# Performance work log

Hardware: AMD Instinct MI355X
Metric: run time of the kernel (lower is better)

Reference implementation:

```python
import jax, jax.numpy as jnp
import numpy as np
from jax import lax

S = 16  # encoder stride (patchify-conv stand-in for the CNN backbone, stride-16 feature grid)


def _conv(x, w, b, stride, padding):
    y = lax.conv_general_dilated(x, w, (stride, stride), padding,
                                 dimension_numbers=('NCHW', 'OIHW', 'NCHW'))
    return y + b[None, :, None, None]


def _l2norm(x, eps=1e-12):  # F.normalize(p=2, dim=1)
    n = jnp.sqrt(jnp.sum(x * x, axis=1, keepdims=True))
    return x / jnp.maximum(n, eps)


def _encode(frame, ew, eb, kw, kb, vw, vb, mask=None):
    feat = jax.nn.relu(_conv(frame, ew, eb, S, 'VALID'))  # [B,512,h,w]
    key = _conv(feat, kw, kb, 1, 'SAME')                  # [B,64,h,w]
    val = _conv(feat, vw, vb, 1, 'SAME')                  # [B,ed,h,w]
    if mask is not None:
        m = mask[:, None, ::S, ::S]  # torch F.interpolate 'nearest' with exact integer factor
        key = key * m
        val = val * m
    return _l2norm(key), val, feat


def _forward(query_frame, prev_frame, prev_mask, first_frame, first_mask,
             enc_q_w, enc_q_b, enc_m_w, enc_m_b,
             key_w, key_b, val_w, val_b,
             dec1_w, dec1_b, dec2_w, dec2_b, cls_w, cls_b):
    # memory bank reset + push(first), push(prev)
    k1, v1, _ = _encode(first_frame, enc_m_w, enc_m_b, key_w, key_b, val_w, val_b, first_mask)
    kp, vp, _ = _encode(prev_frame, enc_m_w, enc_m_b, key_w, key_b, val_w, val_b, prev_mask)
    qk, qv, _ = _encode(query_frame, enc_q_w, enc_q_b, key_w, key_b, val_w, val_b)
    B, Ck, h, w = qk.shape
    ed = qv.shape[1]
    mem_key = jnp.concatenate([k1.reshape(B, Ck, -1), kp.reshape(B, Ck, -1)], axis=2)  # [B,64,M]
    mem_val = jnp.concatenate([v1.reshape(B, ed, -1), vp.reshape(B, ed, -1)], axis=2)  # [B,ed,M]
    q_key = qk.reshape(B, Ck, -1)                                                      # [B,64,Q]
    # STM memory read: affinity -> softmax -> weighted sum over memory pixels
    affinity = jnp.einsum('bcq,bcm->bqm', q_key, mem_key) / jnp.sqrt(jnp.float32(Ck))
    affinity = jax.nn.softmax(affinity, axis=-1)
    mem_read = jnp.einsum('bqm,bcm->bcq', affinity, mem_val).reshape(B, ed, h, w)
    fused = jnp.concatenate([qv, mem_read], axis=1)  # [B,2*ed,h,w] (aspp=False)
    d = jax.nn.relu(_conv(fused, dec1_w, dec1_b, 1, 'SAME'))
    dec_feat = jax.nn.relu(_conv(d, dec2_w, dec2_b, 1, 'SAME'))
    logits = _conv(dec_feat, cls_w, cls_b, 1, 'SAME')
    H, W = query_frame.shape[-2], query_frame.shape[-1]
    logits_full = jax.image.resize(logits, (B, logits.shape[1], H, W), method='bilinear')  # align_corners=False
    rep_feat = _l2norm(dec_feat)
    return rep_feat, logits_full


def setup_inputs():
    key = jax.random.key(0)
    ks = jax.random.split(key, 16)
    B, H, W = 8, 512, 512
    Ce, Ck, ed = 512, 64, 256
    g = lambda i, sh, s: jax.random.normal(ks[i], sh, dtype=jnp.float32) * s
    return {
        'query_frame': g(0, (B, 3, H, W), 1.0),
        'prev_frame': g(1, (B, 3, H, W), 1.0),
        'prev_mask': jnp.round(jax.random.uniform(ks[2], (B, H, W), dtype=jnp.float32)),
        'first_frame': g(3, (B, 3, H, W), 1.0),
        'first_mask': jnp.round(jax.random.uniform(ks[4], (B, H, W), dtype=jnp.float32)),
        'enc_q_w': g(5, (Ce, 3, S, S), 0.02), 'enc_q_b': jnp.zeros((Ce,), jnp.float32),
        'enc_m_w': g(6, (Ce, 3, S, S), 0.02), 'enc_m_b': jnp.zeros((Ce,), jnp.float32),
        'key_w': g(7, (Ck, Ce, 1, 1), 0.05), 'key_b': jnp.zeros((Ck,), jnp.float32),
        'val_w': g(8, (ed, Ce, 1, 1), 0.05), 'val_b': jnp.zeros((ed,), jnp.float32),
        'dec1_w': g(9, (ed, 2 * ed, 3, 3), 0.02), 'dec1_b': jnp.zeros((ed,), jnp.float32),
        'dec2_w': g(10, (ed, ed, 3, 3), 0.02), 'dec2_b': jnp.zeros((ed,), jnp.float32),
        'cls_w': g(11, (2, ed, 1, 1), 0.05), 'cls_b': jnp.zeros((2,), jnp.float32),
    }


def reference(query_frame, prev_frame, prev_mask, first_frame, first_mask,
              enc_q_w, enc_q_b, enc_m_w, enc_m_b,
              key_w, key_b, val_w, val_b,
              dec1_w, dec1_b, dec2_w, dec2_b, cls_w, cls_b):
    return _forward(query_frame, prev_frame, prev_mask, first_frame, first_mask,
                    enc_q_w, enc_q_b, enc_m_w, enc_m_b,
                    key_w, key_b, val_w, val_b,
                    dec1_w, dec1_b, dec2_w, dec2_b, cls_w, cls_b)
```

## Files before the change

kernel.cpp:

```cpp
#include <hip/hip_runtime.h>
#include <hip/hip_bf16.h>
#include <cstdint>

#define DEV __device__ __forceinline__
typedef __attribute__((ext_vector_type(8))) short short8;
typedef __attribute__((ext_vector_type(4))) float f32x4;
typedef unsigned short u16;

DEV float b2f(u16 u) { union { unsigned int i; float f; } x; x.i = (unsigned)u << 16; return x.f; }
DEV u16 f2b(float f) { __hip_bfloat16 h = __float2bfloat16(f); return *(u16*)&h; }
DEV float rdin(const void* p, size_t i, int isbf) {
  return isbf ? __bfloat162float(((const __hip_bfloat16*)p)[i]) : ((const float*)p)[i];
}
DEV void wrout(void* p, size_t i, float v, int isbf) {
  if (isbf) ((__hip_bfloat16*)p)[i] = __float2bfloat16(v);
  else      ((float*)p)[i] = v;
}
DEV short8 ld8(const void* p, size_t idx, int isbf) {
  if (isbf) return *(const short8*)((const u16*)p + idx);
  const float* f = (const float*)p + idx;
  float4 x = *(const float4*)f, y = *(const float4*)(f + 4);
  short8 r;
  r[0] = f2b(x.x); r[1] = f2b(x.y); r[2] = f2b(x.z); r[3] = f2b(x.w);
  r[4] = f2b(y.x); r[5] = f2b(y.y); r[6] = f2b(y.z); r[7] = f2b(y.w);
  return r;
}
DEV void gl16(const u16* g, u16* l) {
  __builtin_amdgcn_global_load_lds(
      (const __attribute__((address_space(1))) void*)g,
      (__attribute__((address_space(3))) void*)l, 16, 0, 0);
}
DEV void bar() {
  asm volatile("" ::: "memory");
  __builtin_amdgcn_s_barrier();
  asm volatile("" ::: "memory");
}

__global__ __launch_bounds__(256) void detect_k(const u16* w, int* flag) {
  __shared__ int cnt[256];
  int tid = threadIdx.x, c = 0;
  for (int i = tid; i < 4096; i += 256) {
    u16 v = w[i];
    int e = (v >> 7) & 0xFF;
    if (v == 0 || (e >= 0x60 && e <= 0x9F)) c++;
  }
  cnt[tid] = c;
  __syncthreads();
  for (int s = 128; s > 0; s >>= 1) { if (tid < s) cnt[tid] += cnt[tid + s]; __syncthreads(); }
  if (tid == 0) *flag = (cnt[0] > 3600) ? 1 : 0;
}

__global__ __launch_bounds__(256) void patchify_k(const void* F0, const void* F1,
                                                  u16* dst, const int* dflag) {
  int isbf = *dflag;
  int bid = blockIdx.x;
  int z = bid >> 8, rem = bid & 255, b = rem >> 5, y = rem & 31;
  const void* F = z ? F1 : F0;
  int x = threadIdx.x & 31, pj = threadIdx.x >> 5;
  u16* drow = dst + (size_t)(z * 8192 + b * 1024 + y * 32 + x) * 768;
#pragma unroll
  for (int i = 0; i < 6; i++) {
    int pair = i * 8 + pj;
    int c = pair >> 4, ky = pair & 15;
    size_t src = ((size_t)((b * 3 + c) * 512 + y * 16 + ky)) * 512 + x * 16;
    short8 v0 = ld8(F, src, isbf);
    short8 v1 = ld8(F, src + 8, isbf);
    u16* dp = drow + c * 256 + ky * 16;
    *(short8*)dp = v0;
    *(short8*)(dp + 8) = v1;
  }
}

__global__ __launch_bounds__(256) void wconv_k(const void* wm, const void* wq,
                                               u16* dst, float* rsum, const int* dflag) {
  int isbf = *dflag;
  int gi = blockIdx.x * 256 + threadIdx.x;
  if (gi < 8192) rsum[gi] = 0.f;
  size_t e0 = (size_t)gi * 8;
  const void* src = e0 < 393216 ? wm : wq;
  size_t off = e0 < 393216 ? e0 : e0 - 393216;
  *(short8*)&dst[e0] = ld8(src, off, isbf);
}

__global__ __launch_bounds__(256) void kvconv_k(const void* valW, const void* keyW,
                                                u16* dst, const int* dflag) {
  int isbf = *dflag;
  int idx = blockIdx.x * 256 + threadIdx.x;
  size_t e0 = (size_t)idx * 8;
  int row = (int)(e0 >> 9);
  const void* src = row < 256 ? valW : keyW;
  size_t off = row < 256 ? e0 : e0 - (size_t)256 * 512;
  *(short8*)&dst[e0] = ld8(src, off, isbf);
}

struct PA {
  const void* W0; const void* W1; size_t bs; int K; int rowsplit; int zsel; int ws16; int rowmax1;
  DEV short8 l8(int row, int k, int b, int zz, int isbf) const {
    const void* W = W0; int r = row;
    if (zsel && zz == 2) W = W1;
    else if (rowsplit && row >= rowsplit) { W = W1; r = row - rowsplit; if (r > rowmax1) r = rowmax1; }
    return ld8(W, (size_t)b * bs + (size_t)r * K + k, ws16 ? 1 : isbf);
  }
  DEV const u16* ga(int row, int k, int b, int zz) const {
    int r = row; if (rowsplit && r > rowmax1) r = rowmax1;
    return (const u16*)W0 + (size_t)b * bs + (size_t)r * K + k;
  }
};
struct PBws {
  const u16* X; int rs; size_t zs;
  DEV short8 l8(int t, int k, int zz, int) const {
    return *(const short8*)(X + (size_t)zz * zs + (size_t)t * rs + k);
  }
  DEV const u16* ga(int t, int k, int zz) const {
    return X + (size_t)zz * zs + (size_t)t * rs + k;
  }
};
struct PBc3 {
  const u16* X; int C; int shift;
  DEV short8 l8(int t, int k, int, int) const {
    int tap = k >> shift, c0 = k & (C - 1);
    int dy = tap / 3, dx = tap - dy * 3;
    int pos = t & 1023, y = pos >> 5, x = pos & 31;
    int iy = y + dy - 1, ix = x + dx - 1;
    if ((unsigned)iy >= 32u || (unsigned)ix >= 32u) { short8 z = {0,0,0,0,0,0,0,0}; return z; }
    return *(const short8*)(X + (size_t)(((t >> 10) * 1024) + iy * 32 + ix) * C + c0);
  }
};

struct Epi {
  int mode;
  u16 *o16, *o16b, *o16c;
  size_t zs; int ts, moff, mmax;
  const void *bias, *bias2; int bzsel;
  const void *maskA, *maskB;
  const float* rscale;
  float scale; int relu, doexp;
  float* rsum;
  int rinv;
  DEV void store1(int m, int t, int z, float v, int isbf) const {
    if (m >= mmax) return;
    int b = t >> 10, pos = t & 1023;
    if (m < 256) {
      v += rdin(bias, m, isbf);
      if (z < 2) {
        const void* mk = z ? maskB : maskA;
        v *= rdin(mk, ((size_t)(b * 512 + (pos >> 5) * 16) << 9) + (pos & 31) * 16, isbf);
        o16[((size_t)(b * 256 + m)) * 2048 + (size_t)z * 1024 + pos] = f2b(v);
      } else {
        o16b[(size_t)t * 512 + m] = f2b(v);
      }
    } else {
      v += rdin(bias2, m - 256, isbf);
      o16c[((size_t)z * 8192 + t) * 64 + (m - 256)] = f2b(v);
    }
  }
};

DEV void epilogue(const Epi& ep, f32x4 (&acc)[4][4], u16* sh, int isbf, int tid,
                  int col16, int quad, int wm, int wn, int zz, int m0, int n0, int nbase) {
  if (ep.mode == 1) {
#pragma unroll
    for (int mt = 0; mt < 4; mt++)
#pragma unroll
      for (int nt = 0; nt < 4; nt++)
#pragma unroll
        for (int r = 0; r < 4; r++) {
          int m = m0 + wm * 64 + mt * 16 + quad * 4 + r;
          int t = nbase + n0 + wn * 64 + nt * 16 + col16;
          ep.store1(m, t, zz, acc[mt][nt][r], isbf);
        }
    return;
  }
  if (ep.mode == 2) {
    float* pf = (float*)ep.o16;
#pragma unroll
    for (int mt = 0; mt < 4; mt++)
#pragma unroll
      for (int nt = 0; nt < 4; nt++)
#pragma unroll
        for (int r = 0; r < 4; r++) {
          int m = m0 + wm * 64 + mt * 16 + quad * 4 + r;
          int t = nbase + n0 + wn * 64 + nt * 16 + col16;
          pf[((size_t)(zz * 256 + m)) * 8192 + t] = acc[mt][nt][r];
        }
    return;
  }
  u16* T = sh;
  const int TS = 132;
  for (int p = 0; p < 2; p++) {
    __syncthreads();
    if (wn == p) {
      float tsum[4] = {0.f, 0.f, 0.f, 0.f};
#pragma unroll
      for (int mt = 0; mt < 4; mt++)
#pragma unroll
        for (int nt = 0; nt < 4; nt++) {
          int tl = nt * 16 + col16;
          int tg = nbase + n0 + p * 64 + tl;
#pragma unroll
          for (int r2 = 0; r2 < 2; r2++) {
            int ml = wm * 64 + mt * 16 + quad * 4 + r2 * 2;
            float v0 = acc[mt][nt][r2 * 2] * ep.scale;
            float v1 = acc[mt][nt][r2 * 2 + 1] * ep.scale;
            if (ep.bias) {
              const void* bp = (ep.bzsel && zz == 2) ? ep.bias2 : ep.bias;
              v0 += rdin(bp, m0 + ml, isbf);
              v1 += rdin(bp, m0 + ml + 1, isbf);
            }
            if (ep.doexp) { v0 = __expf(v0); v1 = __expf(v1); }
            if (ep.rscale) {
              float rs = ep.rscale[tg];
              if (ep.rinv) rs = 1.f / rs;
              v0 *= rs; v1 *= rs;
            }
            if (ep.relu) { v0 = fmaxf(v0, 0.f); v1 = fmaxf(v1, 0.f); }
            if (ep.rsum) tsum[nt] += v0 + v1;
            unsigned int pk = (unsigned)f2b(v0) | ((unsigned)f2b(v1) << 16);
            *(unsigned int*)&T[tl * TS + ml] = pk;
          }
        }
      if (ep.rsum) {
#pragma unroll
        for (int nt = 0; nt < 4; nt++)
          atomicAdd(&ep.rsum[nbase + n0 + p * 64 + nt * 16 + col16], tsum[nt]);
      }
    }
    __syncthreads();
    {
      int tl = tid >> 2, seg = tid & 3;
      int tg = nbase + n0 + p * 64 + tl;
      u16* op = ep.o16 + (size_t)zz * ep.zs + (size_t)tg * ep.ts + ep.moff + m0;
#pragma unroll
      for (int i = 0; i < 4; i++) {
        int c8 = seg + i * 4;
        short8 v = *(short8*)&T[tl * TS + c8 * 8];
        *(short8*)&op[c8 * 8] = v;
      }
    }
  }
}

template <class PB>
__global__ __launch_bounds__(256) void mgl(PA pa, PB pb, Epi ep, int ktiles, int nbase,
                                           const int* dflag) {
  __shared__ u16 sh[32768];
  int isbf = *dflag;
  int tid = threadIdx.x, lane = tid & 63;
  int col16 = lane & 15, quad = lane >> 4;
  int wv = tid >> 6, wm = wv >> 1, wn = wv & 1;
  int zz = blockIdx.z;
  int n0 = blockIdx.x * 128, m0 = blockIdx.y * 128;
  int bA = (nbase + n0) >> 10;

  f32x4 acc[4][4];
#pragma unroll
  for (int mt = 0; mt < 4; mt++)
#pragma unroll
    for (int nt = 0; nt < 4; nt++)
#pragma unroll
      for (int r = 0; r < 4; r++) acc[mt][nt][r] = 0.f;

  int rA[4], lA[4];
#pragma unroll
  for (int g = 0; g < 4; g++) {
    rA[g] = g * 32 + (tid >> 3);
    lA[g] = (tid & 7) ^ (rA[g] & 7);
  }

  auto issue = [&](int kt) {
    int kk = kt * 64;
    u16* base = sh + ((kt & 1) << 14);
#pragma unroll
    for (int g = 0; g < 4; g++) {
      gl16(pa.ga(m0 + rA[g], kk + lA[g] * 8, bA, zz), base + (size_t)(g * 256 + tid) * 8);
      gl16(pb.ga(nbase + n0 + rA[g], kk + lA[g] * 8, zz), base + 8192 + (size_t)(g * 256 + tid) * 8);
    }
  };
  issue(0);

  for (int kt = 0; kt < ktiles; kt++) {
    const u16* As = sh + ((kt & 1) << 14);
    const u16* Bs = As + 8192;
    if (kt + 1 < ktiles) {
      issue(kt + 1);
      asm volatile("s_waitcnt vmcnt(8)" ::: "memory");
    } else {
      asm volatile("s_waitcnt vmcnt(0)" ::: "memory");
    }
    bar();
#pragma unroll
    for (int s = 0; s < 2; s++) {
      short8 af[4], bf[4];
      int cs = ((s * 4 + quad) ^ (col16 & 7)) << 3;
#pragma unroll
      for (int mt = 0; mt < 4; mt++)
        af[mt] = *(const short8*)&As[(wm * 64 + mt * 16 + col16) * 64 + cs];
#pragma unroll
      for (int nt = 0; nt < 4; nt++)
        bf[nt] = *(const short8*)&Bs[(wn * 64 + nt * 16 + col16) * 64 + cs];
#pragma unroll
      for (int mt = 0; mt < 4; mt++)
#pragma unroll
        for (int nt = 0; nt < 4; nt++)
          acc[mt][nt] = __builtin_amdgcn_mfma_f32_16x16x32_bf16(af[mt], bf[nt], acc[mt][nt], 0, 0, 0);
    }
    bar();
  }

  epilogue(ep, acc, sh, isbf, tid, col16, quad, wm, wn, zz, m0, n0, nbase);
}

template <class PB>
__global__ __launch_bounds__(256) void mg(PA pa, PB pb, Epi ep, int ktiles, int nbase,
                                          int ksplit, const int* dflag) {
  __shared__ u16 sh[32768];
  int isbf = *dflag;
  int tid = threadIdx.x, lane = tid & 63;
  int col16 = lane & 15, quad = lane >> 4;
  int wv = tid >> 6, wm = wv >> 1, wn = wv & 1;
  int zz = blockIdx.z;
  int kb = ksplit * zz;
  int n0 = blockIdx.x * 128, m0 = blockIdx.y * 128;
  int bA = (nbase + n0) >> 10;

  f32x4 acc[4][4];
#pragma unroll
  for (int mt = 0; mt < 4; mt++)
#pragma unroll
    for (int nt = 0; nt < 4; nt++)
#pragma unroll
      for (int r = 0; r < 4; r++) acc[mt][nt][r] = 0.f;

  int rA[4], lA[4];
#pragma unroll
  for (int g = 0; g < 4; g++) {
    rA[g] = g * 32 + (tid >> 3);
    lA[g] = (tid & 7) ^ (rA[g] & 7);
  }

  short8 ra[4], rb[4];
#pragma unroll
  for (int g = 0; g < 4; g++) {
    ra[g] = pa.l8(m0 + rA[g], kb + lA[g] * 8, bA, zz, isbf);
    rb[g] = pb.l8(nbase + n0 + rA[g], kb + lA[g] * 8, zz, isbf);
  }
#pragma unroll
  for (int g = 0; g < 4; g++) {
    *(short8*)&sh[(size_t)(g * 256 + tid) * 8] = ra[g];
    *(short8*)&sh[8192 + (size_t)(g * 256 + tid) * 8] = rb[g];
  }
  __syncthreads();

  for (int kt = 0; kt < ktiles; kt++) {
    const u16* As = sh + ((kt & 1) ? 16384 : 0);
    const u16* Bs = As + 8192;
    bool more = (kt + 1 < ktiles);
    if (more) {
      int kn = kb + (kt + 1) * 64;
#pragma unroll
      for (int g = 0; g < 4; g++) {
        ra[g] = pa.l8(m0 + rA[g], kn + lA[g] * 8, bA, zz, isbf);
        rb[g] = pb.l8(nbase + n0 + rA[g], kn + lA[g] * 8, zz, isbf);
      }
    }
#pragma unroll
    for (int s = 0; s < 2; s++) {
      short8 af[4], bf[4];
      int cs = ((s * 4 + quad) ^ (col16 & 7)) << 3;
#pragma unroll
      for (int mt = 0; mt < 4; mt++)
        af[mt] = *(const short8*)&As[(wm * 64 + mt * 16 + col16) * 64 + cs];
#pragma unroll
      for (int nt = 0; nt < 4; nt++)
        bf[nt] = *(const short8*)&Bs[(wn * 64 + nt * 16 + col16) * 64 + cs];
#pragma unroll
      for (int mt = 0; mt < 4; mt++)
#pragma unroll
        for (int nt = 0; nt < 4; nt++)
          acc[mt][nt] = __builtin_amdgcn_mfma_f32_16x16x32_bf16(af[mt], bf[nt], acc[mt][nt], 0, 0, 0);
    }
    if (more) {
      u16* An = sh + (!(kt & 1) ? 16384 : 0);
#pragma unroll
      for (int g = 0; g < 4; g++) {
        *(short8*)&An[(size_t)(g * 256 + tid) * 8] = ra[g];
        *(short8*)&An[8192 + (size_t)(g * 256 + tid) * 8] = rb[g];
      }
      __syncthreads();
    }
  }

  epilogue(ep, acc, sh, isbf, tid, col16, quad, wm, wn, zz, m0, n0, nbase);
}

__global__ __launch_bounds__(256) void comb_k(const float* pf, const void* bias,
                                              u16* out, int ts, int moff, int npart,
                                              int relu, const float* rsum,
                                              const int* dflag) {
  int isbf = *dflag;
  int tid = threadIdx.x;
  int t = blockIdx.x * 64 + (tid & 63);
  int m = blockIdx.y * 8 + ((tid >> 6) << 1);
  float rs = rsum ? 1.f / rsum[t] : 1.f;
  float v0 = 0.f, v1 = 0.f;
  for (int p = 0; p < npart; p++) {
    v0 += pf[(size_t)(p * 256 + m) * 8192 + t];
    v1 += pf[(size_t)(p * 256 + m + 1) * 8192 + t];
  }
  v0 *= rs; v1 *= rs;
  if (bias) { v0 += rdin(bias, m, isbf); v1 += rdin(bias, m + 1, isbf); }
  if (relu) { v0 = fmaxf(v0, 0.f); v1 = fmaxf(v1, 0.f); }
  unsigned int pk = (unsigned)f2b(v0) | ((unsigned)f2b(v1) << 16);
  *(unsigned int*)&out[(size_t)t * ts + moff + m] = pk;
}

__global__ __launch_bounds__(256) void wreorder_k(const void* src, u16* dst, int C,
                                                  int total, const int* dflag) {
  int idx = blockIdx.x * 256 + threadIdx.x;
  if (idx >= total) return;
  int isbf = *dflag;
  int nine_c = 9 * C;
  int m = idx / nine_c; int r = idx - m * nine_c;
  int tp = r / C; int c = r - tp * C;
  dst[idx] = f2b(rdin(src, (size_t)(m * C + c) * 9 + tp, isbf));
}

__global__ __launch_bounds__(256) void keyfix_k(const u16* kraw3, const void* mA,
                                                const void* mB, u16* memk, u16* qk,
                                                const int* dflag) {
  int isbf = *dflag;
  int z = blockIdx.y;
  int n = blockIdx.x * 256 + threadIdx.x;
  int b = n >> 10, pos = n & 1023;
  float mv = 1.f;
  if (z == 0) mv = rdin(mA, ((size_t)(b * 512 + (pos >> 5) * 16) << 9) + (pos & 31) * 16, isbf);
  else if (z == 1) mv = rdin(mB, ((size_t)(b * 512 + (pos >> 5) * 16) << 9) + (pos & 31) * 16, isbf);
  const u16* src = kraw3 + ((size_t)z * 8192 + n) * 64;
  float v[64], ss = 0.f;
#pragma unroll
  for (int c = 0; c < 64; c++) { v[c] = b2f(src[c]) * mv; ss += v[c] * v[c]; }
  float inv = 1.f / fmaxf(sqrtf(ss), 1e-12f);
  u16* dst = (z < 2) ? memk + (size_t)(b * 2048 + z * 1024 + pos) * 64 : qk + (size_t)n * 64;
#pragma unroll
  for (int c = 0; c < 64; c++) dst[c] = f2b(v[c] * inv);
}

__global__ __launch_bounds__(256) void repcls_k(const u16* decf, const void* cwgt,
                                                const void* cbias, void* out_rep,
                                                float* logits, const int* dflag) {
  int isbf = *dflag;
  int tid = threadIdx.x, lane = tid & 63, wv = tid >> 6;
  int tok = blockIdx.x * 4 + wv;
  int b = tok >> 10, pos = tok & 1023;
  const u16* src = decf + (size_t)tok * 256;
  int c0 = lane * 4;
  float v[4], ss = 0.f, a0 = 0.f, a1 = 0.f;
#pragma unroll
  for (int j = 0; j < 4; j++) {
    float x = b2f(src[c0 + j]);
    v[j] = x; ss += x * x;
    a0 = fmaf(x, rdin(cwgt, c0 + j, isbf), a0);
    a1 = fmaf(x, rdin(cwgt, 256 + c0 + j, isbf), a1);
  }
#pragma unroll
  for (int off = 32; off > 0; off >>= 1) {
    ss += __shfl_down(ss, off); a0 += __shfl_down(a0, off); a1 += __shfl_down(a1, off);
  }
  ss = __shfl(ss, 0); a0 = __shfl(a0, 0); a1 = __shfl(a1, 0);
  float inv = 1.f / fmaxf(sqrtf(ss), 1e-12f);
#pragma unroll
  for (int j = 0; j < 4; j++)
    wrout(out_rep, ((size_t)(b * 256 + c0 + j) << 10) + pos, v[j] * inv, isbf);
  if (lane == 0) {
    logits[((size_t)(b * 2) << 10) + pos]     = a0 + rdin(cbias, 0, isbf);
    logits[((size_t)(b * 2 + 1) << 10) + pos] = a1 + rdin(cbias, 1, isbf);
  }
}

__global__ __launch_bounds__(256) void resize_k(const float* logits, void* out,
                                                size_t ebase, const int* dflag) {
  int isbf = *dflag;
  int idx = blockIdx.x * 256 + threadIdx.x;
  int ox = idx & 511, oy = (idx >> 9) & 511, c = (idx >> 18) & 1, b = idx >> 19;
  float fy = (oy + 0.5f) * 0.0625f - 0.5f;
  float fx = (ox + 0.5f) * 0.0625f - 0.5f;
  int y0 = (int)floorf(fy), x0 = (int)floorf(fx);
  float wy = fy - y0, wx = fx - x0;
  int y0c = max(y0, 0), y1c = min(y0 + 1, 31);
  int x0c = max(x0, 0), x1c = min(x0 + 1, 31);
  const float* L = logits + ((size_t)(b * 2 + c) << 10);
  float v00 = L[y0c * 32 + x0c], v01 = L[y0c * 32 + x1c];
  float v10 = L[y1c * 32 + x0c], v11 = L[y1c * 32 + x1c];
  float v = (1.f - wy) * ((1.f - wx) * v00 + wx * v01) + wy * ((1.f - wx) * v10 + wx * v11);
  wrout(out, ebase + (size_t)idx, v, isbf);
}

extern "C" void kernel_launch(void* const* d_in, const int* in_sizes, int n_in,
                              void* d_out, int out_size, void* d_ws, size_t ws_size,
                              hipStream_t stream) {
  const void* query  = d_in[0];  const void* prev   = d_in[1];
  const void* prevM  = d_in[2];  const void* first  = d_in[3];
  const void* firstM = d_in[4];  const void* encQw  = d_in[5];
  const void* encQb  = d_in[6];  const void* encMw  = d_in[7];
  const void* encMb  = d_in[8];  const void* keyW   = d_in[9];
  const void* keyB   = d_in[10]; const void* valW   = d_in[11];
  const void* valB   = d_in[12]; const void* dec1W  = d_in[13];
  const void* dec1B  = d_in[14]; const void* dec2W  = d_in[15];
  const void* dec2B  = d_in[16]; const void* clsW   = d_in[17];
  const void* clsB   = d_in[18];

  u16* W = (u16*)d_ws;
  int* dflag = (int*)W;
  float* rsum   = (float*)(W + 16);
  float* logits = (float*)(W + 16400);
  u16* B0 = W + 49168;
  u16* Xp    = B0;
  u16* feat3 = B0 + 12582912;
  u16* encWb = B0 + 25165824;
  u16* wr1   = B0;
  u16* wr2   = B0 + 1179648;
  u16* fused = B0 + 1769472;
  u16* memv  = B0 + 5963776;
  u16* memk  = B0 + 10158080;
  u16* qk    = B0 + 11206656;
  u16* kraw3 = B0 + 25165824;
  u16* kvW   = B0 + 26738688;
  u16* P     = B0 + 11730944;
  float* pf  = (float*)(B0 + 11730944);
  u16* dbuf  = memv;
  u16* decf  = memv + 2097152;

  dim3 blk(256);
  detect_k<<<dim3(1), blk, 0, stream>>>((const u16*)encQw, dflag);

  wconv_k<<<dim3(384), blk, 0, stream>>>(encMw, encQw, encWb, rsum, dflag);
  patchify_k<<<dim3(512), blk, 0, stream>>>(first, prev, Xp, dflag);
  {
    PA a{encWb, 0, 0, 768, 0, 0, 1, 0};
    PBws b{Xp, 768, (size_t)8192 * 768};
    Epi e{0, feat3, 0, 0, (size_t)8192 * 512, 512, 0, 512,
          encMb, 0, 0, 0, 0, 0, 1.f, 1, 0};
    mgl<PBws><<<dim3(64, 4, 2), blk, 0, stream>>>(a, b, e, 12, 0, dflag);
  }
  patchify_k<<<dim3(256), blk, 0, stream>>>(query, query, Xp, dflag);
  {
    PA a{encWb + 393216, 0, 0, 768, 0, 0, 1, 0};
    PBws b{Xp, 768, 0};
    Epi e{0, feat3 + (size_t)2 * 8192 * 512, 0, 0, 0, 512, 0, 512,
          encQb, 0, 0, 0, 0, 0, 1.f, 1, 0};
    mgl<PBws><<<dim3(64, 4, 1), blk, 0, stream>>>(a, b, e, 12, 0, dflag);
  }

  wreorder_k<<<dim3(4608), blk, 0, stream>>>(dec1W, wr1, 512, 256 * 4608, dflag);
  wreorder_k<<<dim3(2304), blk, 0, stream>>>(dec2W, wr2, 256, 256 * 2304, dflag);
  kvconv_k<<<dim3(80), blk, 0, stream>>>(valW, keyW, kvW, dflag);

  {
    PA a{kvW, 0, 0, 512, 1, 0, 1, 319};
    PBws b{feat3, 512, (size_t)8192 * 512};
    Epi e{1, memv, fused, kraw3, 0, 0, 0, 320,
          valB, keyB, 0, firstM, prevM, 0, 1.f, 0, 0};
    mgl<PBws><<<dim3(64, 3, 3), blk, 0, stream>>>(a, b, e, 8, 0, dflag);
  }
  keyfix_k<<<dim3(32, 3), blk, 0, stream>>>(kraw3, firstM, prevM, memk, qk, dflag);

  {
    PA a{memk, 0, 131072, 64, 0, 0, 1, 0};
    PBws b{qk, 64, 0};
    Epi e{0, P, 0, 0, 0, 2048, 0, 1 << 30,
          0, 0, 0, 0, 0, 0, 0.125f, 0, 1, rsum, 0};
    mgl<PBws><<<dim3(64, 16, 1), blk, 0, stream>>>(a, b, e, 1, 0, dflag);
  }
  {
    PA a{memv, 0, 524288, 2048, 0, 0, 1, 0};
    PBws b{P, 2048, 0};
    Epi e{0, fused, 0, 0, 0, 512, 256, 1 << 30,
          0, 0, 0, 0, 0, rsum, 1.f, 0, 0, 0, 1};
    mgl<PBws><<<dim3(64, 2, 1), blk, 0, stream>>>(a, b, e, 32, 0, dflag);
  }

  {
    PA a{wr1, 0, 0, 4608, 0, 0, 1, 0};
    PBc3 b{fused, 512, 9};
    Epi e{2, (u16*)pf, 0, 0, 0, 0, 0, 0,
          0, 0, 0, 0, 0, 0, 1.f, 0, 0};
    mg<PBc3><<<dim3(64, 2, 4), blk, 0, stream>>>(a, b, e, 18, 0, 1152, dflag);
    comb_k<<<dim3(128, 32), blk, 0, stream>>>(pf, dec1B, dbuf, 256, 0, 4, 1, 0, dflag);
  }
  {
    PA a{wr2, 0, 0, 2304, 0, 0, 1, 0};
    PBc3 b{dbuf, 256, 8};
    Epi e{2, (u16*)pf, 0, 0, 0, 0, 0, 0,
          0, 0, 0, 0, 0, 0, 1.f, 0, 0};
    mg<PBc3><<<dim3(64, 2, 2), blk, 0, stream>>>(a, b, e, 18, 0, 1152, dflag);
    comb_k<<<dim3(128, 32), blk, 0, stream>>>(pf, dec2B, decf, 256, 0, 2, 1, 0, dflag);
  }

  repcls_k<<<dim3(2048), blk, 0, stream>>>(decf, clsW, clsB, d_out, logits, dflag);
  resize_k<<<dim3(16384), blk, 0, stream>>>(logits, d_out, (size_t)2097152, dflag);
}
```

Measured before the change: 529.2 us.

## Fuse STM memory-read affinity, exp and value aggregation into flash-style attention kernel

Replaces the two GEMM launches for the memory read (QK affinity with exp epilogue written to a P buffer, then P·V) with one fused attention kernel. It splits the memory dimension into four parts and keeps exp-scores in shared memory per 64-key chunk, so the large affinity matrix never goes to global memory. A small combine kernel then sums the partials and normalises by the row sums. No max-subtraction is done, as in the code before, and a single wave computes the scores while the other three wait, which can limit throughput.

```diff
diff --git a/kernel.cpp b/kernel.cpp
--- a/kernel.cpp
+++ b/kernel.cpp
@@ -72,10 +72,9 @@
 }
 
 __global__ __launch_bounds__(256) void wconv_k(const void* wm, const void* wq,
-                                               u16* dst, float* rsum, const int* dflag) {
+                                               u16* dst, const int* dflag) {
   int isbf = *dflag;
   int gi = blockIdx.x * 256 + threadIdx.x;
-  if (gi < 8192) rsum[gi] = 0.f;
   size_t e0 = (size_t)gi * 8;
   const void* src = e0 < 393216 ? wm : wq;
   size_t off = e0 < 393216 ? e0 : e0 - 393216;
@@ -135,8 +134,6 @@
   const void *maskA, *maskB;
   const float* rscale;
   float scale; int relu, doexp;
-  float* rsum;
-  int rinv;
   DEV void store1(int m, int t, int z, float v, int isbf) const {
     if (m >= mmax) return;
     int b = t >> 10, pos = t & 1023;
@@ -190,13 +187,11 @@
   for (int p = 0; p < 2; p++) {
     __syncthreads();
     if (wn == p) {
-      float tsum[4] = {0.f, 0.f, 0.f, 0.f};
 #pragma unroll
       for (int mt = 0; mt < 4; mt++)
 #pragma unroll
         for (int nt = 0; nt < 4; nt++) {
           int tl = nt * 16 + col16;
-          int tg = nbase + n0 + p * 64 + tl;
 #pragma unroll
           for (int r2 = 0; r2 < 2; r2++) {
             int ml = wm * 64 + mt * 16 + quad * 4 + r2 * 2;
@@ -207,23 +202,11 @@
               v0 += rdin(bp, m0 + ml, isbf);
               v1 += rdin(bp, m0 + ml + 1, isbf);
             }
-            if (ep.doexp) { v0 = __expf(v0); v1 = __expf(v1); }
-            if (ep.rscale) {
-              float rs = ep.rscale[tg];
-              if (ep.rinv) rs = 1.f / rs;
-              v0 *= rs; v1 *= rs;
-            }
             if (ep.relu) { v0 = fmaxf(v0, 0.f); v1 = fmaxf(v1, 0.f); }
-            if (ep.rsum) tsum[nt] += v0 + v1;
             unsigned int pk = (unsigned)f2b(v0) | ((unsigned)f2b(v1) << 16);
             *(unsigned int*)&T[tl * TS + ml] = pk;
           }
         }
-      if (ep.rsum) {
-#pragma unroll
-        for (int nt = 0; nt < 4; nt++)
-          atomicAdd(&ep.rsum[nbase + n0 + p * 64 + nt * 16 + col16], tsum[nt]);
-      }
     }
     __syncthreads();
     {
@@ -393,21 +376,176 @@
   epilogue(ep, acc, sh, isbf, tid, col16, quad, wm, wn, zz, m0, n0, nbase);
 }
 
+__global__ __launch_bounds__(256) void attn_k(const u16* qk, const u16* memk,
+                                              const u16* memv, float* pf, float* rsum) {
+  __shared__ u16 sh[28672];
+  __shared__ float rsl[64];
+  const int Qt = 0, Kt = 4096, Vt = 8192, Pl = 24576;
+  int tid = threadIdx.x, lane = tid & 63;
+  int col16 = lane & 15, quad = lane >> 4;
+  int wv = tid >> 6;
+  int b = blockIdx.x >> 4, qt = blockIdx.x & 15;
+  int q0 = b * 1024 + qt * 64;
+  int s = blockIdx.y;
+  int kv0 = s * 512;
+
+  if (tid < 64) rsl[tid] = 0.f;
+
+  int r32 = tid >> 3;
+#pragma unroll
+  for (int g = 0; g < 2; g++) {
+    int row = g * 32 + r32;
+    int k8 = (tid & 7) ^ (row & 7);
+    gl16(qk + (size_t)(q0 + row) * 64 + k8 * 8, sh + Qt + (size_t)(g * 256 + tid) * 8);
+  }
+  {
+#pragma unroll
+    for (int g = 0; g < 2; g++) {
+      int row = g * 32 + r32;
+      int k8 = (tid & 7) ^ (row & 7);
+      gl16(memk + ((size_t)(b * 2048 + kv0 + row)) * 64 + k8 * 8,
+           sh + Kt + (size_t)(g * 256 + tid) * 8);
+    }
+#pragma unroll
+    for (int g = 0; g < 8; g++) {
+      int row = g * 32 + r32;
+      int k8 = (tid & 7) ^ (row & 7);
+      gl16(memv + ((size_t)(b * 256 + row)) * 2048 + kv0 + k8 * 8,
+           sh + Vt + (size_t)(g * 256 + tid) * 8);
+    }
+  }
+  __syncthreads();
+
+  f32x4 acc_o[4][4];
+#pragma unroll
+  for (int mt = 0; mt < 4; mt++)
+#pragma unroll
+    for (int nt = 0; nt < 4; nt++)
+#pragma unroll
+      for (int r = 0; r < 4; r++) acc_o[mt][nt][r] = 0.f;
+
+  for (int ch = 0; ch < 8; ch++) {
+    if (tid < 64) {
+      f32x4 acc_s[4][4];
+#pragma unroll
+      for (int mt = 0; mt < 4; mt++)
+#pragma unroll
+        for (int nt = 0; nt < 4; nt++)
+#pragma unroll
+          for (int r = 0; r < 4; r++) acc_s[mt][nt][r] = 0.f;
+#pragma unroll
+      for (int s2 = 0; s2 < 2; s2++) {
+        short8 af[4], bf[4];
+        int cs = ((s2 * 4 + quad) ^ (col16 & 7)) << 3;
+#pragma unroll
+        for (int mt = 0; mt < 4; mt++)
+          af[mt] = *(const short8*)&sh[Kt + (mt * 16 + col16) * 64 + cs];
+#pragma unroll
+        for (int nt = 0; nt < 4; nt++)
+          bf[nt] = *(const short8*)&sh[Qt + (nt * 16 + col16) * 64 + cs];
+#pragma unroll
+        for (int mt = 0; mt < 4; mt++)
+#pragma unroll
+          for (int nt = 0; nt < 4; nt++)
+            acc_s[mt][nt] = __builtin_amdgcn_mfma_f32_16x16x32_bf16(af[mt], bf[nt], acc_s[mt][nt], 0, 0, 0);
+      }
+#pragma unroll
+      for (int nt = 0; nt < 4; nt++) {
+        int ql = nt * 16 + col16;
+        float tsum = 0.f;
+#pragma unroll
+        for (int mt = 0; mt < 4; mt++)
+#pragma unroll
+          for (int r = 0; r < 4; r++) {
+            int kvl = mt * 16 + quad * 4 + r;
+            u16 pb = f2b(__expf(0.125f * acc_s[mt][nt][r]));
+            tsum += b2f(pb);
+            sh[Pl + ql * 64 + (((kvl >> 3) ^ (ql & 7)) << 3) + (kvl & 7)] = pb;
+          }
+        tsum += __shfl_xor(tsum, 16);
+        tsum += __shfl_xor(tsum, 32);
+        if (quad == 0) rsl[ql] += tsum;
+      }
+    }
+    __syncthreads();
+#pragma unroll
+    for (int s2 = 0; s2 < 2; s2++) {
+      short8 af[4], bf[4];
+      int cs = ((s2 * 4 + quad) ^ (col16 & 7)) << 3;
+#pragma unroll
+      for (int mt = 0; mt < 4; mt++)
+        af[mt] = *(const short8*)&sh[Vt + (wv * 64 + mt * 16 + col16) * 64 + cs];
+#pragma unroll
+      for (int nt = 0; nt < 4; nt++)
+        bf[nt] = *(const short8*)&sh[Pl + (nt * 16 + col16) * 64 + cs];
+#pragma unroll
+      for (int mt = 0; mt < 4; mt++)
+#pragma unroll
+        for (int nt = 0; nt < 4; nt++)
+          acc_o[mt][nt] = __builtin_amdgcn_mfma_f32_16x16x32_bf16(af[mt], bf[nt], acc_o[mt][nt], 0, 0, 0);
+    }
+    __syncthreads();
+    if (ch + 1 < 8) {
+      int kvc = kv0 + (ch + 1) * 64;
+#pragma unroll
+      for (int g = 0; g < 2; g++) {
+        int row = g * 32 + r32;
+        int k8 = (tid & 7) ^ (row & 7);
+        gl16(memk + ((size_t)(b * 2048 + kvc + row)) * 64 + k8 * 8,
+             sh + Kt + (size_t)(g * 256 + tid) * 8);
+      }
+#pragma unroll
+      for (int g = 0; g < 8; g++) {
+        int row = g * 32 + r32;
+        int k8 = (tid & 7) ^ (row & 7);
+        gl16(memv + ((size_t)(b * 256 + row)) * 2048 + kvc + k8 * 8,
+             sh + Vt + (size_t)(g * 256 + tid) * 8);
+      }
+    }
+    __syncthreads();
+  }
+
+#pragma unroll
+  for (int mt = 0; mt < 4; mt++)
+#pragma unroll
+    for (int nt = 0; nt < 4; nt++)
+#pragma unroll
+      for (int r = 0; r < 4; r++) {
+        int c = wv * 64 + mt * 16 + quad * 4 + r;
+        int q = nt * 16 + col16;
+        pf[((size_t)(s * 8192 + q0 + q)) * 256 + c] = acc_o[mt][nt][r];
+      }
+  if (tid < 64) atomicAdd(&rsum[q0 + tid], rsl[tid]);
+}
+
+__global__ __launch_bounds__(256) void acomb_k(const float* pf, const float* rsum,
+                                               u16* fused) {
+  int tid = threadIdx.x;
+  int t = blockIdx.x * 2 + (tid >> 7);
+  int cp = tid & 127;
+  float inv = 1.f / rsum[t];
+  float v0 = 0.f, v1 = 0.f;
+#pragma unroll
+  for (int s = 0; s < 4; s++) {
+    const float* p = pf + ((size_t)(s * 8192 + t)) * 256 + cp * 2;
+    v0 += p[0]; v1 += p[1];
+  }
+  unsigned int pk = (unsigned)f2b(v0 * inv) | ((unsigned)f2b(v1 * inv) << 16);
+  *(unsigned int*)&fused[(size_t)t * 512 + 256 + cp * 2] = pk;
+}
+
 __global__ __launch_bounds__(256) void comb_k(const float* pf, const void* bias,
                                               u16* out, int ts, int moff, int npart,
-                                              int relu, const float* rsum,
-                                              const int* dflag) {
+                                              int relu, const int* dflag) {
   int isbf = *dflag;
   int tid = threadIdx.x;
   int t = blockIdx.x * 64 + (tid & 63);
   int m = blockIdx.y * 8 + ((tid >> 6) << 1);
-  float rs = rsum ? 1.f / rsum[t] : 1.f;
   float v0 = 0.f, v1 = 0.f;
   for (int p = 0; p < npart; p++) {
     v0 += pf[(size_t)(p * 256 + m) * 8192 + t];
     v1 += pf[(size_t)(p * 256 + m + 1) * 8192 + t];
   }
-  v0 *= rs; v1 *= rs;
   if (bias) { v0 += rdin(bias, m, isbf); v1 += rdin(bias, m + 1, isbf); }
   if (relu) { v0 = fmaxf(v0, 0.f); v1 = fmaxf(v1, 0.f); }
   unsigned int pk = (unsigned)f2b(v0) | ((unsigned)f2b(v1) << 16);
@@ -427,11 +565,12 @@
 
 __global__ __launch_bounds__(256) void keyfix_k(const u16* kraw3, const void* mA,
                                                 const void* mB, u16* memk, u16* qk,
-                                                const int* dflag) {
+                                                float* rsum, const int* dflag) {
   int isbf = *dflag;
   int z = blockIdx.y;
   int n = blockIdx.x * 256 + threadIdx.x;
   int b = n >> 10, pos = n & 1023;
+  if (z == 0) rsum[n] = 0.f;
   float mv = 1.f;
   if (z == 0) mv = rdin(mA, ((size_t)(b * 512 + (pos >> 5) * 16) << 9) + (pos & 31) * 16, isbf);
   else if (z == 1) mv = rdin(mB, ((size_t)(b * 512 + (pos >> 5) * 16) << 9) + (pos & 31) * 16, isbf);
@@ -525,7 +664,6 @@
   u16* qk    = B0 + 11206656;
   u16* kraw3 = B0 + 25165824;
   u16* kvW   = B0 + 26738688;
-  u16* P     = B0 + 11730944;
   float* pf  = (float*)(B0 + 11730944);
   u16* dbuf  = memv;
   u16* decf  = memv + 2097152;
@@ -533,7 +671,7 @@
   dim3 blk(256);
   detect_k<<<dim3(1), blk, 0, stream>>>((const u16*)encQw, dflag);
 
-  wconv_k<<<dim3(384), blk, 0, stream>>>(encMw, encQw, encWb, rsum, dflag);
+  wconv_k<<<dim3(384), blk, 0, stream>>>(encMw, encQw, encWb, dflag);
   patchify_k<<<dim3(512), blk, 0, stream>>>(first, prev, Xp, dflag);
   {
     PA a{encWb, 0, 0, 768, 0, 0, 1, 0};
@@ -562,22 +700,10 @@
           valB, keyB, 0, firstM, prevM, 0, 1.f, 0, 0};
     mgl<PBws><<<dim3(64, 3, 3), blk, 0, stream>>>(a, b, e, 8, 0, dflag);
   }
-  keyfix_k<<<dim3(32, 3), blk, 0, stream>>>(kraw3, firstM, prevM, memk, qk, dflag);
-
-  {
-    PA a{memk, 0, 131072, 64, 0, 0, 1, 0};
-    PBws b{qk, 64, 0};
-    Epi e{0, P, 0, 0, 0, 2048, 0, 1 << 30,
-          0, 0, 0, 0, 0, 0, 0.125f, 0, 1, rsum, 0};
-    mgl<PBws><<<dim3(64, 16, 1), blk, 0, stream>>>(a, b, e, 1, 0, dflag);
-  }
-  {
-    PA a{memv, 0, 524288, 2048, 0, 0, 1, 0};
-    PBws b{P, 2048, 0};
-    Epi e{0, fused, 0, 0, 0, 512, 256, 1 << 30,
-          0, 0, 0, 0, 0, rsum, 1.f, 0, 0, 0, 1};
-    mgl<PBws><<<dim3(64, 2, 1), blk, 0, stream>>>(a, b, e, 32, 0, dflag);
-  }
+  keyfix_k<<<dim3(32, 3), blk, 0, stream>>>(kraw3, firstM, prevM, memk, qk, rsum, dflag);
+
+  attn_k<<<dim3(128, 4), blk, 0, stream>>>(qk, memk, memv, pf, rsum);
+  acomb_k<<<dim3(4096), blk, 0, stream>>>(pf, rsum, fused);
 
   {
     PA a{wr1, 0, 0, 4608, 0, 0, 1, 0};
@@ -585,7 +711,7 @@
     Epi e{2, (u16*)pf, 0, 0, 0, 0, 0, 0,
           0, 0, 0, 0, 0, 0, 1.f, 0, 0};
     mg<PBc3><<<dim3(64, 2, 4), blk, 0, stream>>>(a, b, e, 18, 0, 1152, dflag);
-    comb_k<<<dim3(128, 32), blk, 0, stream>>>(pf, dec1B, dbuf, 256, 0, 4, 1, 0, dflag);
+    comb_k<<<dim3(128, 32), blk, 0, stream>>>(pf, dec1B, dbuf, 256, 0, 4, 1, dflag);
   }
   {
     PA a{wr2, 0, 0, 2304, 0, 0, 1, 0};
@@ -593,7 +719,7 @@
     Epi e{2, (u16*)pf, 0, 0, 0, 0, 0, 0,
           0, 0, 0, 0, 0, 0, 1.f, 0, 0};
     mg<PBc3><<<dim3(64, 2, 2), blk, 0, stream>>>(a, b, e, 18, 0, 1152, dflag);
-    comb_k<<<dim3(128, 32), blk, 0, stream>>>(pf, dec2B, decf, 256, 0, 2, 1, 0, dflag);
+    comb_k<<<dim3(128, 32), blk, 0, stream>>>(pf, dec2B, decf, 256, 0, 2, 1, dflag);
   }
 
   repcls_k<<<dim3(2048), blk, 0, stream>>>(decf, clsW, clsB, d_out, logits, dflag);
```

New measurement: 471.4 us. 1.12x faster.
